# Kernel optimization log

Measured on AMD Instinct MI355X. Metric: run time of the kernel, lower is better.

## Reference

```python
import jax, jax.numpy as jnp
import numpy as np

B, S, D, F = 4, 4096, 1024, 256


def _ln(x, g, b, eps=1e-5):
    m = x.mean(-1, keepdims=True)
    v = ((x - m) ** 2).mean(-1, keepdims=True)
    return (x - m) / jnp.sqrt(v + eps) * g + b


def setup_inputs() -> dict:
    key = jax.random.key(0)
    ks = jax.random.split(key, 8)
    return {
        "x": jax.random.normal(ks[0], (B, S, D), jnp.float32),
        "W_to": jax.random.normal(ks[1], (2 * F, D), jnp.float32) * 0.02,   # to_spectral.weight [out,in]
        "log_decay": jnp.zeros((F,), jnp.float32),
        "frequencies": jax.random.normal(ks[2], (F,), jnp.float32) * 0.01,
        "W_from": jax.random.normal(ks[3], (D, 2 * F), jnp.float32) * 0.02,  # from_spectral.weight
        "ln1_g": jnp.ones((D,), jnp.float32), "ln1_b": jnp.zeros((D,), jnp.float32),
        "ln3_g": jnp.ones((D,), jnp.float32), "ln3_b": jnp.zeros((D,), jnp.float32),
        "W_ffn1": jax.random.normal(ks[4], (4 * D, D), jnp.float32) * 0.02,
        "b_ffn1": jnp.zeros((4 * D,), jnp.float32),
        "W_ffn2": jax.random.normal(ks[5], (D, 4 * D), jnp.float32) * 0.02,
        "b_ffn2": jnp.zeros((D,), jnp.float32),
    }


def reference(x, W_to, log_decay, frequencies, W_from, ln1_g, ln1_b,
              ln3_g, ln3_b, W_ffn1, b_ffn1, W_ffn2, b_ffn2):
    Bc, Sc, Dc = x.shape
    Fc = log_decay.shape[0]
    dt = 1.0  # registered buffer dt = 1.0

    residual = x
    h = _ln(x, ln1_g, ln1_b)
    spec = jnp.einsum('bsd,fd->bsf', h, W_to)          # [B,S,2F]
    real, imag = spec[..., :Fc], spec[..., Fc:]

    decay = jax.nn.sigmoid(log_decay)                   # [F]
    omega = jnp.tanh(frequencies) * 0.1
    c, s = jnp.cos(omega * dt), jnp.sin(omega * dt)

    def step(carry, u):
        sr, si = carry
        r, i = u                                        # [B,F]
        sr = sr * decay + r * 0.1
        si = si * decay + i * 0.1
        nr = jnp.clip(sr * c - si * s, -10.0, 10.0)
        ni = jnp.clip(sr * s + si * c, -10.0, 10.0)
        return (nr, ni), (nr, ni)

    init = (jnp.zeros((Bc, Fc), x.dtype), jnp.zeros((Bc, Fc), x.dtype))
    _, (out_r, out_i) = jax.lax.scan(
        step, init, (real.transpose(1, 0, 2), imag.transpose(1, 0, 2)))
    spectral_out = jnp.concatenate(
        [out_r.transpose(1, 0, 2), out_i.transpose(1, 0, 2)], axis=-1)  # [B,S,2F]

    h = jnp.einsum('bsf,df->bsd', spectral_out, W_from)
    x2 = residual + h * 0.1

    # FFN block (dropout = identity in eval)
    r3 = x2
    h = _ln(x2, ln3_g, ln3_b)
    h = jnp.einsum('bsd,ed->bse', h, W_ffn1) + b_ffn1
    h = jax.nn.gelu(h, approximate=False)               # nn.GELU default = exact erf
    h = jnp.einsum('bse,de->bsd', h, W_ffn2) + b_ffn2
    return r3 + h * 0.1
```

## Files before the change

kernel.cpp:

```cpp
#include <hip/hip_runtime.h>
#include <hip/hip_bf16.h>
#include <math.h>

typedef _Float16 f16x8 __attribute__((ext_vector_type(8)));
typedef _Float16 f16x4 __attribute__((ext_vector_type(4)));
typedef float f32x4 __attribute__((ext_vector_type(4)));
typedef float f32x16 __attribute__((ext_vector_type(16)));
typedef int v4i __attribute__((ext_vector_type(4)));
typedef int v8i __attribute__((ext_vector_type(8)));

#define GAS __attribute__((address_space(1)))
#define LAS __attribute__((address_space(3)))

__device__ __forceinline__ void async_load16(const void* g, void* l) {
  __builtin_amdgcn_global_load_lds((const GAS void*)g, (LAS void*)l, 16, 0, 0);
}

__device__ __forceinline__ float fast_gelu(float x) {
  float x3 = x * x * x;
  float u = 0.7978845608f * x + 0.0356774081f * x3;
  float e = __expf(2.0f * u);
  float t = 1.0f - 2.0f / (e + 1.0f);
  return 0.5f * x * (1.0f + t);
}

__device__ __forceinline__ int pack4_fp8(float a, float b, float c, float d) {
  int p = __builtin_amdgcn_cvt_pk_fp8_f32(a, b, 0, false);
  p = __builtin_amdgcn_cvt_pk_fp8_f32(c, d, p, true);
  return p;
}

__global__ __launch_bounds__(256) void cvt_f16_kernel(const float* __restrict__ in,
                                                      _Float16* __restrict__ out, int n) {
  int i = (blockIdx.x * 256 + threadIdx.x) * 4;
  if (i < n) {
    float4 v = *(const float4*)(in + i);
    f16x4 o;
    o.x = (_Float16)v.x; o.y = (_Float16)v.y; o.z = (_Float16)v.z; o.w = (_Float16)v.w;
    *(f16x4*)(out + i) = o;
  }
}

__global__ __launch_bounds__(256) void cvt_fp8_kernel(const float* __restrict__ in,
                                                      unsigned char* __restrict__ out, int n) {
  int i = (blockIdx.x * 256 + threadIdx.x) * 4;
  if (i < n) {
    float4 v = *(const float4*)(in + i);
    *(int*)(out + i) = pack4_fp8(v.x, v.y, v.z, v.w);
  }
}

__global__ __launch_bounds__(256) void cvt_fp8_perm_kernel(const float* __restrict__ in,
                                                           unsigned char* __restrict__ out) {
  int id = blockIdx.x * 256 + threadIdx.x;
  int n = id >> 10;
  int p0 = (id & 1023) * 4;
  int p7 = p0 & 127;
  int grp = (p7 >> 2) & 3;
  int h = (p7 >> 4) & 1;
  int k_src = (p0 & ~127) | (p7 & 96) | (grp << 3) | (h << 2);
  float4 v = *(const float4*)(in + (size_t)n * 4096 + k_src);
  *(int*)(out + (size_t)n * 4096 + p0) = pack4_fp8(v.x, v.y, v.z, v.w);
}

template <int OUT8>
__global__ __launch_bounds__(256) void ln_kernel(const float* __restrict__ x,
                                                 const float* __restrict__ gamma,
                                                 const float* __restrict__ beta,
                                                 _Float16* __restrict__ outH,
                                                 unsigned char* __restrict__ outB) {
  int row = blockIdx.x;
  int t = threadIdx.x;
  float4 v = ((const float4*)(x + (size_t)row * 1024))[t];
  float s = v.x + v.y + v.z + v.w;
  float s2 = v.x * v.x + v.y * v.y + v.z * v.z + v.w * v.w;
#pragma unroll
  for (int o = 32; o > 0; o >>= 1) { s += __shfl_xor(s, o); s2 += __shfl_xor(s2, o); }
  __shared__ float red[8];
  int w = t >> 6;
  if ((t & 63) == 0) { red[w] = s; red[4 + w] = s2; }
  __syncthreads();
  s = red[0] + red[1] + red[2] + red[3];
  s2 = red[4] + red[5] + red[6] + red[7];
  float mean = s * (1.0f / 1024.0f);
  float var = s2 * (1.0f / 1024.0f) - mean * mean;
  float rstd = rsqrtf(var + 1e-5f);
  float4 gv = ((const float4*)gamma)[t];
  float4 bv = ((const float4*)beta)[t];
  float y0 = (v.x - mean) * rstd * gv.x + bv.x;
  float y1 = (v.y - mean) * rstd * gv.y + bv.y;
  float y2 = (v.z - mean) * rstd * gv.z + bv.z;
  float y3 = (v.w - mean) * rstd * gv.w + bv.w;
  if (OUT8) {
    *(int*)(outB + (size_t)row * 1024 + t * 4) = pack4_fp8(y0, y1, y2, y3);
  } else {
    f16x4 o;
    o.x = (_Float16)y0; o.y = (_Float16)y1; o.z = (_Float16)y2; o.w = (_Float16)y3;
    *(f16x4*)(outH + (size_t)row * 1024 + t * 4) = o;
  }
}

#define SCAN_CH 64
#define SCAN_W 64
__global__ __launch_bounds__(256) void scan_kernel(const _Float16* __restrict__ spec,
                                                   const float* __restrict__ log_decay,
                                                   const float* __restrict__ freq,
                                                   _Float16* __restrict__ so) {
  const int S = 4096;
  const int nchunks = S / SCAN_CH;
  int f = threadIdx.x;
  int b = blockIdx.x / nchunks;
  int ck = blockIdx.x % nchunks;
  int t0 = ck * SCAN_CH;
  int ts = (ck == 0) ? 0 : (t0 - SCAN_W);
  int nsteps = t0 + SCAN_CH - ts;

  float decay = 1.0f / (1.0f + expf(-log_decay[f]));
  float om = tanhf(freq[f]) * 0.1f;
  float co = cosf(om);
  float sn = sinf(om);
  float sr = 0.0f, si = 0.0f;

  const _Float16* base = spec + (size_t)b * S * 512;
  _Float16* ob = so + (size_t)b * S * 512;

  float rb[8], ib[8];
#pragma unroll
  for (int j = 0; j < 8; j++) {
    rb[j] = (float)base[(size_t)(ts + j) * 512 + f];
    ib[j] = (float)base[(size_t)(ts + j) * 512 + 256 + f];
  }
  for (int gs = 0; gs < nsteps; gs += 8) {
    float cr[8], ci[8];
#pragma unroll
    for (int j = 0; j < 8; j++) { cr[j] = rb[j]; ci[j] = ib[j]; }
    if (gs + 8 < nsteps) {
      int nx = ts + gs + 8;
#pragma unroll
      for (int j = 0; j < 8; j++) {
        rb[j] = (float)base[(size_t)(nx + j) * 512 + f];
        ib[j] = (float)base[(size_t)(nx + j) * 512 + 256 + f];
      }
    }
#pragma unroll
    for (int j = 0; j < 8; j++) {
      int t = ts + gs + j;
      sr = sr * decay + cr[j] * 0.1f;
      si = si * decay + ci[j] * 0.1f;
      float nr = sr * co - si * sn;
      float ni = sr * sn + si * co;
      nr = fminf(10.0f, fmaxf(-10.0f, nr));
      ni = fminf(10.0f, fmaxf(-10.0f, ni));
      sr = nr; si = ni;
      if (t >= t0) {
        ob[(size_t)t * 512 + f] = (_Float16)nr;
        ob[(size_t)t * 512 + 256 + f] = (_Float16)ni;
      }
    }
  }
}

template <int EPI>
__global__ __launch_bounds__(256, 2) void gemm_nt_kernel(
    const _Float16* __restrict__ A, const _Float16* __restrict__ Bm,
    const float* __restrict__ bias, const float* resid,
    float* outF, _Float16* __restrict__ outH,
    int M, int N, int K, int lda, int ldb) {
  __shared__ __align__(16) _Float16 As[128 * 32];
  __shared__ __align__(16) _Float16 Bs[128 * 32];
  const int tid = threadIdx.x;
  const int lane = tid & 63;
  const int wave = tid >> 6;
  const int wm = (wave >> 1) * 64;
  const int wn = (wave & 1) * 64;
  const int bm = blockIdx.x * 128;
  const int bn = blockIdx.y * 128;

  size_t ga[2], gb[2];
  int lo[2];
#pragma unroll
  for (int rep = 0; rep < 2; rep++) {
    int lsi = tid + rep * 256;
    int row = lsi >> 2;
    int slot = lsi & 3;
    int sw = (row ^ (row >> 2)) & 3;
    int gseg = slot ^ sw;
    lo[rep] = lsi * 8;
    ga[rep] = (size_t)(bm + row) * lda + (size_t)gseg * 8;
    gb[rep] = (size_t)(bn + row) * ldb + (size_t)gseg * 8;
  }

  const int q = lane >> 4;
  const int ml = lane & 15;
  int aaddr[4], baddr[4];
#pragma unroll
  for (int i = 0; i < 4; i++) {
    int r = wm + i * 16 + ml;
    aaddr[i] = (r * 4 + (q ^ ((r ^ (r >> 2)) & 3))) * 8;
    int rn = wn + i * 16 + ml;
    baddr[i] = (rn * 4 + (q ^ ((rn ^ (rn >> 2)) & 3))) * 8;
  }

  const f32x4 zero = {0.0f, 0.0f, 0.0f, 0.0f};
  f32x4 acc[4][4];
#pragma unroll
  for (int i = 0; i < 4; i++)
#pragma unroll
    for (int j = 0; j < 4; j++) acc[i][j] = zero;

  for (int k0 = 0; k0 < K; k0 += 32) {
    __syncthreads();
#pragma unroll
    for (int rep = 0; rep < 2; rep++) {
      async_load16(A + ga[rep] + k0, As + lo[rep]);
      async_load16(Bm + gb[rep] + k0, Bs + lo[rep]);
    }
    __syncthreads();
    f16x8 af[4], bf[4];
#pragma unroll
    for (int i = 0; i < 4; i++) {
      af[i] = *(const f16x8*)(As + aaddr[i]);
      bf[i] = *(const f16x8*)(Bs + baddr[i]);
    }
#pragma unroll
    for (int i = 0; i < 4; i++)
#pragma unroll
      for (int j = 0; j < 4; j++)
        acc[i][j] = __builtin_amdgcn_mfma_f32_16x16x32_f16(bf[j], af[i], acc[i][j], 0, 0, 0);
  }

#pragma unroll
  for (int i = 0; i < 4; i++) {
    int gm = bm + wm + i * 16 + ml;
#pragma unroll
    for (int j = 0; j < 4; j++) {
      int gn = bn + wn + j * 16 + q * 4;
      size_t idx = (size_t)gm * N + gn;
      f32x4 c = acc[i][j];
      if (EPI == 0) {
        f16x4 o;
        o.x = (_Float16)c[0]; o.y = (_Float16)c[1];
        o.z = (_Float16)c[2]; o.w = (_Float16)c[3];
        *(f16x4*)(outH + idx) = o;
      } else {
        float4 rv = *(const float4*)(resid + idx);
        float4 bv = bias ? *(const float4*)(bias + gn) : float4{0.f, 0.f, 0.f, 0.f};
        float4 o;
        o.x = rv.x + 0.1f * (c[0] + bv.x);
        o.y = rv.y + 0.1f * (c[1] + bv.y);
        o.z = rv.z + 0.1f * (c[2] + bv.z);
        o.w = rv.w + 0.1f * (c[3] + bv.w);
        *(float4*)(outF + idx) = o;
      }
    }
  }
}

template <int EPI>
__global__ __launch_bounds__(512, 2) void gemm_fp8_kernel(
    const unsigned char* __restrict__ A, const unsigned char* __restrict__ Bm,
    const float* __restrict__ bias, const float* resid,
    float* outF, unsigned char* __restrict__ outB,
    int M, int N, int K, int lda, int ldb) {
  __shared__ __align__(16) unsigned char As[4][256 * 64];
  __shared__ __align__(16) unsigned char Bs[4][256 * 64];
  const int tid = threadIdx.x;
  const int lane = tid & 63;
  const int wave = tid >> 6;
  const int wm = (wave >> 2) * 128;
  const int wn = (wave & 3) * 64;
  const int bm = blockIdx.x * 256;
  const int bn = blockIdx.y * 256;

  size_t ga[2], gb[2];
  int lo[2];
#pragma unroll
  for (int rep = 0; rep < 2; rep++) {
    int lsi = tid + rep * 512;
    int row = lsi >> 2;
    int slot = lsi & 3;
    int sw = (row ^ (row >> 2)) & 3;
    int gseg = slot ^ sw;
    lo[rep] = lsi * 16;
    ga[rep] = (size_t)(bm + row) * lda + (size_t)gseg * 16;
    gb[rep] = (size_t)(bn + row) * ldb + (size_t)gseg * 16;
  }

  const int ml = lane & 31;
  const int h2 = lane >> 5;
  int aaddr[4][2], baddr[2][2];
#pragma unroll
  for (int i = 0; i < 4; i++) {
    int r = wm + i * 32 + ml;
    int sw = (r ^ (r >> 2)) & 3;
    aaddr[i][0] = (r * 4 + ((2 * h2) ^ sw)) * 16;
    aaddr[i][1] = (r * 4 + ((2 * h2 + 1) ^ sw)) * 16;
  }
#pragma unroll
  for (int j = 0; j < 2; j++) {
    int rn = wn + j * 32 + ml;
    int sw = (rn ^ (rn >> 2)) & 3;
    baddr[j][0] = (rn * 4 + ((2 * h2) ^ sw)) * 16;
    baddr[j][1] = (rn * 4 + ((2 * h2 + 1) ^ sw)) * 16;
  }

  f32x16 acc[4][2];
#pragma unroll
  for (int i = 0; i < 4; i++)
#pragma unroll
    for (int j = 0; j < 2; j++)
#pragma unroll
      for (int r = 0; r < 16; r++) acc[i][j][r] = 0.0f;

  const int NT = K >> 6;

#define STAGE_T(s, t)                                                       \
  {                                                                         \
    _Pragma("unroll")                                                       \
    for (int rep = 0; rep < 2; rep++) {                                     \
      async_load16(A + ga[rep] + (size_t)(t) * 64, &As[s][lo[rep]]);        \
      async_load16(Bm + gb[rep] + (size_t)(t) * 64, &Bs[s][lo[rep]]);       \
    }                                                                       \
  }

#define COMPUTE_T(s)                                                        \
  {                                                                         \
    v8i af[4], bf[2];                                                       \
    _Pragma("unroll")                                                       \
    for (int i = 0; i < 4; i++) {                                           \
      v4i* ap = (v4i*)&af[i];                                               \
      ap[0] = *(const v4i*)(As[s] + aaddr[i][0]);                           \
      ap[1] = *(const v4i*)(As[s] + aaddr[i][1]);                           \
    }                                                                       \
    _Pragma("unroll")                                                       \
    for (int j = 0; j < 2; j++) {                                           \
      v4i* bp = (v4i*)&bf[j];                                               \
      bp[0] = *(const v4i*)(Bs[s] + baddr[j][0]);                           \
      bp[1] = *(const v4i*)(Bs[s] + baddr[j][1]);                           \
    }                                                                       \
    __builtin_amdgcn_s_setprio(1);                                          \
    _Pragma("unroll")                                                       \
    for (int i = 0; i < 4; i++) {                                           \
      _Pragma("unroll")                                                     \
      for (int j = 0; j < 2; j++)                                           \
        acc[i][j] = __builtin_amdgcn_mfma_scale_f32_32x32x64_f8f6f4(        \
            bf[j], af[i], acc[i][j], 0, 0, 0, 0x7F7F7F7F, 0, 0x7F7F7F7F);   \
    }                                                                       \
    __builtin_amdgcn_s_setprio(0);                                          \
  }

#define SYNC_T(vmc)                                                         \
  asm volatile("s_waitcnt vmcnt(" #vmc ") lgkmcnt(0)" ::: "memory");        \
  __builtin_amdgcn_sched_barrier(0);                                        \
  __builtin_amdgcn_s_barrier();

  STAGE_T(0, 0)
  STAGE_T(1, 1)
  STAGE_T(2, 2)
  SYNC_T(8)

  for (int t4 = 0; t4 + 8 <= NT; t4 += 4) {
#pragma unroll
    for (int u = 0; u < 4; u++) {
      STAGE_T((u + 3) & 3, t4 + u + 3)
      COMPUTE_T(u)
      SYNC_T(8)
    }
  }

  STAGE_T(3, NT - 1)
  COMPUTE_T(0)
  SYNC_T(8)
  COMPUTE_T(1)
  SYNC_T(4)
  COMPUTE_T(2)
  SYNC_T(0)
  COMPUTE_T(3)

#undef STAGE_T
#undef COMPUTE_T
#undef SYNC_T

#pragma unroll
  for (int i = 0; i < 4; i++) {
    int gm = bm + wm + i * 32 + ml;
#pragma unroll
    for (int j = 0; j < 2; j++) {
      if (EPI == 2) {
        int w[4];
#pragma unroll
        for (int grp = 0; grp < 4; grp++) {
          int n0 = bn + wn + j * 32 + grp * 8 + h2 * 4;
          float4 bv = *(const float4*)(bias + n0);
          float v0 = fast_gelu(acc[i][j][grp * 4 + 0] + bv.x);
          float v1 = fast_gelu(acc[i][j][grp * 4 + 1] + bv.y);
          float v2 = fast_gelu(acc[i][j][grp * 4 + 2] + bv.z);
          float v3 = fast_gelu(acc[i][j][grp * 4 + 3] + bv.w);
          w[grp] = pack4_fp8(v0, v1, v2, v3);
        }
        int pbase = bn + wn + j * 32 + h2 * 16;
        v4i pk = {w[0], w[1], w[2], w[3]};
        *(v4i*)(outB + (size_t)gm * N + pbase) = pk;
      } else {
#pragma unroll
        for (int grp = 0; grp < 4; grp++) {
          int n0 = bn + wn + j * 32 + grp * 8 + h2 * 4;
          size_t idx = (size_t)gm * N + n0;
          float4 rv = *(const float4*)(resid + idx);
          float4 bv = *(const float4*)(bias + n0);
          float4 o;
          o.x = rv.x + 0.1f * (acc[i][j][grp * 4 + 0] + bv.x);
          o.y = rv.y + 0.1f * (acc[i][j][grp * 4 + 1] + bv.y);
          o.z = rv.z + 0.1f * (acc[i][j][grp * 4 + 2] + bv.z);
          o.w = rv.w + 0.1f * (acc[i][j][grp * 4 + 3] + bv.w);
          *(float4*)(outF + idx) = o;
        }
      }
    }
  }
}

extern "C" void kernel_launch(void* const* d_in, const int* in_sizes, int n_in,
                              void* d_out, int out_size, void* d_ws, size_t ws_size,
                              hipStream_t stream) {
  const int Bb = 4, S = 4096, D = 1024, F = 256;
  const int M = Bb * S;
  const int N1 = 2 * F;
  const int NF = 4 * D;

  const float* x       = (const float*)d_in[0];
  const float* W_to    = (const float*)d_in[1];
  const float* log_dec = (const float*)d_in[2];
  const float* freq    = (const float*)d_in[3];
  const float* W_from  = (const float*)d_in[4];
  const float* ln1_g   = (const float*)d_in[5];
  const float* ln1_b   = (const float*)d_in[6];
  const float* ln3_g   = (const float*)d_in[7];
  const float* ln3_b   = (const float*)d_in[8];
  const float* W_ffn1  = (const float*)d_in[9];
  const float* b_ffn1  = (const float*)d_in[10];
  const float* W_ffn2  = (const float*)d_in[11];
  const float* b_ffn2  = (const float*)d_in[12];
  float* out = (float*)d_out;
  (void)in_sizes; (void)n_in; (void)out_size; (void)ws_size;

  char* ws = (char*)d_ws;
  _Float16*      Wto_h   = (_Float16*)(ws);
  _Float16*      Wfrom_h = (_Float16*)(ws + (size_t)1048576);
  unsigned char* Wf1_8   = (unsigned char*)(ws + (size_t)2097152);
  unsigned char* Wf2_8   = (unsigned char*)(ws + (size_t)6291456);
  char* dyn = ws + (size_t)10485760;
  _Float16*      h16     = (_Float16*)(dyn);
  _Float16*      so      = (_Float16*)(dyn);
  _Float16*      spec16  = (_Float16*)(dyn + (size_t)33554432);
  unsigned char* h8      = (unsigned char*)(dyn + (size_t)50331648);
  unsigned char* g8      = (unsigned char*)(dyn + (size_t)67108864);

  cvt_f16_kernel<<<(N1 * D) / 1024, 256, 0, stream>>>(W_to, Wto_h, N1 * D);
  cvt_f16_kernel<<<(D * N1) / 1024, 256, 0, stream>>>(W_from, Wfrom_h, D * N1);
  cvt_fp8_kernel<<<(NF * D) / 1024, 256, 0, stream>>>(W_ffn1, Wf1_8, NF * D);
  cvt_fp8_perm_kernel<<<(D * NF) / 1024, 256, 0, stream>>>(W_ffn2, Wf2_8);

  ln_kernel<0><<<M, 256, 0, stream>>>(x, ln1_g, ln1_b, h16, nullptr);

  gemm_nt_kernel<0><<<dim3(M / 128, N1 / 128), 256, 0, stream>>>(
      h16, Wto_h, nullptr, nullptr, nullptr, spec16, M, N1, D, D, D);

  scan_kernel<<<Bb * (S / SCAN_CH), 256, 0, stream>>>(spec16, log_dec, freq, so);

  gemm_nt_kernel<1><<<dim3(M / 128, D / 128), 256, 0, stream>>>(
      so, Wfrom_h, nullptr, x, out, nullptr, M, D, N1, N1, N1);

  ln_kernel<1><<<M, 256, 0, stream>>>(out, ln3_g, ln3_b, nullptr, h8);

  gemm_fp8_kernel<2><<<dim3(M / 256, NF / 256), 512, 0, stream>>>(
      h8, Wf1_8, b_ffn1, nullptr, nullptr, g8, M, NF, D, D, D);

  gemm_fp8_kernel<1><<<dim3(M / 256, D / 256), 512, 0, stream>>>(
      g8, Wf2_8, b_ffn2, out, out, nullptr, M, D, NF, NF, NF);
}
```

Measured before the change: 511.7 us.

## Merge weight conversions into one launch, deepen fp16 GEMM K-step, relax fp8 bounds

The four weight-conversion kernels become a single launch that branches on thread index, which removes three kernel launches and their tails. The fp16 NT GEMM now stages two 32-wide K slices per barrier pair (64 per iteration), halving the number of sync points at the cost of twice the LDS. The fp8 GEMM's launch bounds drop from two blocks per CU to one, which lets the compiler use more registers but may reduce occupancy.

```diff
diff --git a/kernel.cpp b/kernel.cpp
--- a/kernel.cpp
+++ b/kernel.cpp
@@ -30,37 +30,39 @@
   return p;
 }
 
-__global__ __launch_bounds__(256) void cvt_f16_kernel(const float* __restrict__ in,
-                                                      _Float16* __restrict__ out, int n) {
-  int i = (blockIdx.x * 256 + threadIdx.x) * 4;
-  if (i < n) {
-    float4 v = *(const float4*)(in + i);
+__global__ __launch_bounds__(256) void cvt_all_kernel(
+    const float* __restrict__ W_to, const float* __restrict__ W_from,
+    const float* __restrict__ W_ffn1, const float* __restrict__ W_ffn2,
+    _Float16* __restrict__ Wto_h, _Float16* __restrict__ Wfrom_h,
+    unsigned char* __restrict__ Wf1_8, unsigned char* __restrict__ Wf2_8) {
+  int id = blockIdx.x * 256 + threadIdx.x;
+  if (id < 131072) {
+    int i = id * 4;
+    float4 v = *(const float4*)(W_to + i);
     f16x4 o;
     o.x = (_Float16)v.x; o.y = (_Float16)v.y; o.z = (_Float16)v.z; o.w = (_Float16)v.w;
-    *(f16x4*)(out + i) = o;
-  }
-}
-
-__global__ __launch_bounds__(256) void cvt_fp8_kernel(const float* __restrict__ in,
-                                                      unsigned char* __restrict__ out, int n) {
-  int i = (blockIdx.x * 256 + threadIdx.x) * 4;
-  if (i < n) {
-    float4 v = *(const float4*)(in + i);
-    *(int*)(out + i) = pack4_fp8(v.x, v.y, v.z, v.w);
-  }
-}
-
-__global__ __launch_bounds__(256) void cvt_fp8_perm_kernel(const float* __restrict__ in,
-                                                           unsigned char* __restrict__ out) {
-  int id = blockIdx.x * 256 + threadIdx.x;
-  int n = id >> 10;
-  int p0 = (id & 1023) * 4;
-  int p7 = p0 & 127;
-  int grp = (p7 >> 2) & 3;
-  int h = (p7 >> 4) & 1;
-  int k_src = (p0 & ~127) | (p7 & 96) | (grp << 3) | (h << 2);
-  float4 v = *(const float4*)(in + (size_t)n * 4096 + k_src);
-  *(int*)(out + (size_t)n * 4096 + p0) = pack4_fp8(v.x, v.y, v.z, v.w);
+    *(f16x4*)(Wto_h + i) = o;
+  } else if (id < 262144) {
+    int i = (id - 131072) * 4;
+    float4 v = *(const float4*)(W_from + i);
+    f16x4 o;
+    o.x = (_Float16)v.x; o.y = (_Float16)v.y; o.z = (_Float16)v.z; o.w = (_Float16)v.w;
+    *(f16x4*)(Wfrom_h + i) = o;
+  } else if (id < 1310720) {
+    int i = (id - 262144) * 4;
+    float4 v = *(const float4*)(W_ffn1 + i);
+    *(int*)(Wf1_8 + i) = pack4_fp8(v.x, v.y, v.z, v.w);
+  } else {
+    int id2 = id - 1310720;
+    int n = id2 >> 10;
+    int p0 = (id2 & 1023) * 4;
+    int p7 = p0 & 127;
+    int grp = (p7 >> 2) & 3;
+    int h = (p7 >> 4) & 1;
+    int k_src = (p0 & ~127) | (p7 & 96) | (grp << 3) | (h << 2);
+    float4 v = *(const float4*)(W_ffn2 + (size_t)n * 4096 + k_src);
+    *(int*)(Wf2_8 + (size_t)n * 4096 + p0) = pack4_fp8(v.x, v.y, v.z, v.w);
+  }
 }
 
 template <int OUT8>
@@ -166,8 +168,8 @@
     const float* __restrict__ bias, const float* resid,
     float* outF, _Float16* __restrict__ outH,
     int M, int N, int K, int lda, int ldb) {
-  __shared__ __align__(16) _Float16 As[128 * 32];
-  __shared__ __align__(16) _Float16 Bs[128 * 32];
+  __shared__ __align__(16) _Float16 As[2][128 * 32];
+  __shared__ __align__(16) _Float16 Bs[2][128 * 32];
   const int tid = threadIdx.x;
   const int lane = tid & 63;
   const int wave = tid >> 6;
@@ -208,25 +210,31 @@
 #pragma unroll
     for (int j = 0; j < 4; j++) acc[i][j] = zero;
 
-  for (int k0 = 0; k0 < K; k0 += 32) {
+  for (int k0 = 0; k0 < K; k0 += 64) {
     __syncthreads();
 #pragma unroll
-    for (int rep = 0; rep < 2; rep++) {
-      async_load16(A + ga[rep] + k0, As + lo[rep]);
-      async_load16(Bm + gb[rep] + k0, Bs + lo[rep]);
+    for (int h = 0; h < 2; h++) {
+#pragma unroll
+      for (int rep = 0; rep < 2; rep++) {
+        async_load16(A + ga[rep] + k0 + h * 32, &As[h][lo[rep]]);
+        async_load16(Bm + gb[rep] + k0 + h * 32, &Bs[h][lo[rep]]);
+      }
     }
     __syncthreads();
-    f16x8 af[4], bf[4];
-#pragma unroll
-    for (int i = 0; i < 4; i++) {
-      af[i] = *(const f16x8*)(As + aaddr[i]);
-      bf[i] = *(const f16x8*)(Bs + baddr[i]);
-    }
-#pragma unroll
-    for (int i = 0; i < 4; i++)
-#pragma unroll
-      for (int j = 0; j < 4; j++)
-        acc[i][j] = __builtin_amdgcn_mfma_f32_16x16x32_f16(bf[j], af[i], acc[i][j], 0, 0, 0);
+#pragma unroll
+    for (int h = 0; h < 2; h++) {
+      f16x8 af[4], bf[4];
+#pragma unroll
+      for (int i = 0; i < 4; i++) {
+        af[i] = *(const f16x8*)(As[h] + aaddr[i]);
+        bf[i] = *(const f16x8*)(Bs[h] + baddr[i]);
+      }
+#pragma unroll
+      for (int i = 0; i < 4; i++)
+#pragma unroll
+        for (int j = 0; j < 4; j++)
+          acc[i][j] = __builtin_amdgcn_mfma_f32_16x16x32_f16(bf[j], af[i], acc[i][j], 0, 0, 0);
+    }
   }
 
 #pragma unroll
@@ -257,7 +265,7 @@
 }
 
 template <int EPI>
-__global__ __launch_bounds__(512, 2) void gemm_fp8_kernel(
+__global__ __launch_bounds__(512, 1) void gemm_fp8_kernel(
     const unsigned char* __restrict__ A, const unsigned char* __restrict__ Bm,
     const float* __restrict__ bias, const float* resid,
     float* outF, unsigned char* __restrict__ outB,
@@ -456,10 +464,8 @@
   unsigned char* h8      = (unsigned char*)(dyn + (size_t)50331648);
   unsigned char* g8      = (unsigned char*)(dyn + (size_t)67108864);
 
-  cvt_f16_kernel<<<(N1 * D) / 1024, 256, 0, stream>>>(W_to, Wto_h, N1 * D);
-  cvt_f16_kernel<<<(D * N1) / 1024, 256, 0, stream>>>(W_from, Wfrom_h, D * N1);
-  cvt_fp8_kernel<<<(NF * D) / 1024, 256, 0, stream>>>(W_ffn1, Wf1_8, NF * D);
-  cvt_fp8_perm_kernel<<<(D * NF) / 1024, 256, 0, stream>>>(W_ffn2, Wf2_8);
+  cvt_all_kernel<<<9216, 256, 0, stream>>>(W_to, W_from, W_ffn1, W_ffn2,
+                                           Wto_h, Wfrom_h, Wf1_8, Wf2_8);
 
   ln_kernel<0><<<M, 256, 0, stream>>>(x, ln1_g, ln1_b, h16, nullptr);
 
```

Measured after the change: 502.9 us. No clear change (-1.7%).
